# Kernel tuning notes

Hardware: AMD Instinct MI355X
Metric: run time of the kernel (lower is better)

## Reference

```python
import jax, jax.numpy as jnp
import numpy as np

T, C, H, W = 4, 512, 14, 14
NH, HD, N = 8, 64, H * W  # heads, head_dim, tokens
EPS = 1e-5
SG_ALPHA = 4.0  # spikingjelly default sigmoid surrogate alpha


@jax.custom_vjp
def heaviside_sg(u):
    return (u >= 0.0).astype(u.dtype)

def _hs_fwd(u):
    return heaviside_sg(u), u

def _hs_bwd(u, g):
    s = jax.nn.sigmoid(SG_ALPHA * u)
    return (g * SG_ALPHA * s * (1.0 - s),)

heaviside_sg.defvjp(_hs_fwd, _hs_bwd)


def lif(x, tau=2.0, v_th=1.0):
    """Multi-step LIF over leading time dim; hard reset to 0, detach_reset."""
    def step(v, xt):
        v = v + (xt - v) / tau
        s = heaviside_sg(v - v_th)
        v = v * (1.0 - jax.lax.stop_gradient(s))
        return v, s
    _, spikes = jax.lax.scan(step, jnp.zeros_like(x[0]), x)
    return spikes


def conv1x1_bn(x, w, gamma, beta, mean, var, bias=None):
    # x: [T,C,H,W]; 1x1 conv == channel matmul, then eval-mode BN
    y = jnp.einsum('tchw,oc->tohw', x, w)
    if bias is not None:
        y = y + bias[None, :, None, None]
    scale = gamma / jnp.sqrt(var + EPS)
    return y * scale[None, :, None, None] + (beta - mean * scale)[None, :, None, None]


def to_heads(y):
    # [T,C,H,W] -> [T, NH, N, HD]
    return y.reshape(T, C, N).transpose(0, 2, 1).reshape(T, N, NH, HD).transpose(0, 2, 1, 3)


def setup_inputs() -> dict:
    key = jax.random.key(0)
    ks = jax.random.split(key, 6)
    d = {
        'x': jax.random.normal(ks[0], (T, C, H, W), jnp.float32),
        'q_w': jax.random.normal(ks[1], (C, C), jnp.float32) * 0.05,
        'k_w': jax.random.normal(ks[2], (C, C), jnp.float32) * 0.05,
        'v_w': jax.random.normal(ks[3], (C, C), jnp.float32) * 0.05,
        'proj_w': jax.random.normal(ks[4], (C, C), jnp.float32) * 0.05,
        'proj_b': jnp.zeros((C,), jnp.float32),
    }
    for p in ('q', 'k', 'v', 'proj'):
        d[p + '_gamma'] = jnp.ones((C,), jnp.float32)
        d[p + '_beta'] = jnp.zeros((C,), jnp.float32)
        d[p + '_mean'] = jnp.zeros((C,), jnp.float32)
        d[p + '_var'] = jnp.ones((C,), jnp.float32)
    return d


def reference(x, q_w, q_gamma, q_beta, q_mean, q_var,
              k_w, k_gamma, k_beta, k_mean, k_var,
              v_w, v_gamma, v_beta, v_mean, v_var,
              proj_w, proj_b, proj_gamma, proj_beta, proj_mean, proj_var):
    identity = x
    xs = lif(x)  # shortcut_lif

    q = to_heads(lif(conv1x1_bn(xs, q_w, q_gamma, q_beta, q_mean, q_var)))  # [T,NH,N,HD]
    k = to_heads(lif(conv1x1_bn(xs, k_w, k_gamma, k_beta, k_mean, k_var)))
    v = to_heads(lif(conv1x1_bn(xs, v_w, v_gamma, v_beta, v_mean, v_var)))

    kv = (k * v).sum(axis=2, keepdims=True)        # [T,NH,1,HD] linear attention reduce
    kv = lif(kv, v_th=0.5)                          # talking_heads_lif
    attn = q * kv                                   # [T,NH,N,HD]

    y = attn.transpose(0, 1, 3, 2).reshape(T, C, H, W)
    out = conv1x1_bn(y, proj_w, proj_gamma, proj_beta, proj_mean, proj_var, bias=proj_b)
    return out + identity
```

## Files before the change

kernel.cpp:

```cpp
#include <hip/hip_runtime.h>


#define TT 4
#define CC 512
#define NN 196
#define BEPS 1e-5f

#define WQT_OFF 0
#define WKT_OFF (512 * 512)
#define WVT_OFF (2 * 512 * 512)
#define WPT_OFF (3 * 512 * 512)
#define KV_OFF  (4 * 512 * 512)
#define SQ_OFF  (4 * 512 * 512 + 2048)

__global__ __launch_bounds__(256) void k0_prep(
    const float* __restrict__ qw, const float* __restrict__ kw,
    const float* __restrict__ vw, const float* __restrict__ pw,
    float* __restrict__ ws)
{
    __shared__ float tile[64][65];
    const int b   = blockIdx.x;
    const int mat = b >> 6;
    const int t6  = b & 63;
    const int to  = (t6 >> 3) * 64;
    const int tc  = (t6 & 7) * 64;
    const float* W = (mat == 0) ? qw : (mat == 1) ? kw : (mat == 2) ? vw : pw;
    float* Wt = ws + (size_t)mat * (512 * 512);
    const int lr = threadIdx.x >> 6;
    const int lc = threadIdx.x & 63;
#pragma unroll
    for (int i = 0; i < 16; ++i) {
        int r = i * 4 + lr;
        tile[r][lc] = W[(size_t)(to + r) * 512 + (tc + lc)];
    }
    __syncthreads();
#pragma unroll
    for (int i = 0; i < 16; ++i) {
        int r = i * 4 + lr;
        Wt[(size_t)(tc + r) * 512 + (to + lc)] = tile[lc][r];
    }
    if (b == 0) {
        for (int i = threadIdx.x; i < TT * CC; i += 256) ws[KV_OFF + i] = 0.0f;
    }
}

__device__ __forceinline__ int bn_lif4(const float* acc, float sc, float of, float vth) {
    float v = 0.0f;
    int bits = 0;
#pragma unroll
    for (int t = 0; t < TT; ++t) {
        float y = acc[t] * sc + of;
        v = v + (y - v) * 0.5f;
        if (v >= vth) { bits |= (1 << t); v = 0.0f; }
    }
    return bits;
}

__device__ __forceinline__ void compact_append(int flag, int ch, int lane,
                                               unsigned short* actrow, int* cntp)
{
    unsigned long long m = __ballot(flag);
    int base = 0;
    if (lane == 0 && m) base = atomicAdd(cntp, __popcll(m));
    base = __shfl(base, 0);
    if (flag) actrow[base + __popcll(m & ((1ull << lane) - 1ull))] = (unsigned short)ch;
}

__global__ __launch_bounds__(512) void ka_qkv(
    const float* __restrict__ x, float* __restrict__ ws,
    const float* __restrict__ qg, const float* __restrict__ qb,
    const float* __restrict__ qm, const float* __restrict__ qv,
    const float* __restrict__ kg, const float* __restrict__ kb,
    const float* __restrict__ km, const float* __restrict__ kvv,
    const float* __restrict__ vg, const float* __restrict__ vb,
    const float* __restrict__ vm, const float* __restrict__ vvv)
{
    const int n    = blockIdx.x;
    const int tid  = threadIdx.x;
    const int lane = tid & 63;
    const int wave = tid >> 6;
    __shared__ unsigned short act[TT][CC];
    __shared__ int cnt[TT];
    if (tid < TT) cnt[tid] = 0;

    int xf = 0;
    {
        float v = 0.0f;
#pragma unroll
        for (int t = 0; t < TT; ++t) {
            float a = x[(size_t)(t * CC + tid) * NN + n];
            v = v + (a - v) * 0.5f;
            if (v >= 1.0f) { xf |= (1 << t); v = 0.0f; }
        }
    }
    __syncthreads();
#pragma unroll
    for (int t = 0; t < TT; ++t)
        compact_append((xf >> t) & 1, tid, lane, act[t], &cnt[t]);
    __syncthreads();

    int ct[TT];
    int mc = 0;
#pragma unroll
    for (int t = 0; t < TT; ++t) { ct[t] = cnt[t]; mc = max(mc, ct[t]); }

    float aq[TT] = {0,0,0,0}, ak[TT] = {0,0,0,0}, av[TT] = {0,0,0,0};
    const float* Wqt = ws + WQT_OFF;
    const float* Wkt = ws + WKT_OFF;
    const float* Wvt = ws + WVT_OFF;
    for (int i = 0; i < mc; ++i) {
#pragma unroll
        for (int t = 0; t < TT; ++t) {
            if (i < ct[t]) {
                const int c = act[t][i];
                aq[t] += Wqt[(size_t)c * CC + tid];
                ak[t] += Wkt[(size_t)c * CC + tid];
                av[t] += Wvt[(size_t)c * CC + tid];
            }
        }
    }

    int sqb, skb, svb;
    {
        float sc = qg[tid] / sqrtf(qv[tid] + BEPS);
        sqb = bn_lif4(aq, sc, qb[tid] - qm[tid] * sc, 1.0f);
        sc = kg[tid] / sqrtf(kvv[tid] + BEPS);
        skb = bn_lif4(ak, sc, kb[tid] - km[tid] * sc, 1.0f);
        sc = vg[tid] / sqrtf(vvv[tid] + BEPS);
        svb = bn_lif4(av, sc, vb[tid] - vm[tid] * sc, 1.0f);
    }

    unsigned* sqg = (unsigned*)(ws + SQ_OFF);
    float* kvsum = ws + KV_OFF;
#pragma unroll
    for (int t = 0; t < TT; ++t) {
        unsigned long long m = __ballot((sqb >> t) & 1);
        if (lane == 0) {
            sqg[((size_t)t * NN + n) * 16 + wave * 2]     = (unsigned)(m & 0xffffffffULL);
            sqg[((size_t)t * NN + n) * 16 + wave * 2 + 1] = (unsigned)(m >> 32);
        }
        if (((skb >> t) & 1) && ((svb >> t) & 1)) atomicAdd(&kvsum[t * CC + tid], 1.0f);
    }
}

__global__ __launch_bounds__(512) void kb_proj(
    const float* __restrict__ x, const float* __restrict__ ws,
    const float* __restrict__ pbias,
    const float* __restrict__ pg, const float* __restrict__ pb,
    const float* __restrict__ pm, const float* __restrict__ pv,
    float* __restrict__ out)
{
    const int n    = blockIdx.x;
    const int tid  = threadIdx.x;
    const int lane = tid & 63;
    __shared__ unsigned short act[TT][CC];
    __shared__ int cnt[TT];
    if (tid < TT) cnt[tid] = 0;

    const float* kvsum = ws + KV_OFF;
    const unsigned* sqg = (const unsigned*)(ws + SQ_OFF);

    int f = 0;
    {
        float v = 0.0f;
#pragma unroll
        for (int t = 0; t < TT; ++t) {
            float a = kvsum[t * CC + tid];
            v = v + (a - v) * 0.5f;
            const int s = (v >= 0.5f);
            if (s) v = 0.0f;
            const unsigned w = sqg[((size_t)t * NN + n) * 16 + (tid >> 5)];
            if (s && ((w >> (tid & 31)) & 1)) f |= (1 << t);
        }
    }
    __syncthreads();
#pragma unroll
    for (int t = 0; t < TT; ++t)
        compact_append((f >> t) & 1, tid, lane, act[t], &cnt[t]);
    __syncthreads();

    int ct[TT];
    int mc = 0;
#pragma unroll
    for (int t = 0; t < TT; ++t) { ct[t] = cnt[t]; mc = max(mc, ct[t]); }

    float a[TT] = {0,0,0,0};
    const float* Wpt = ws + WPT_OFF;
    for (int i = 0; i < mc; ++i) {
#pragma unroll
        for (int t = 0; t < TT; ++t) {
            if (i < ct[t]) {
                const int c = act[t][i];
                a[t] += Wpt[(size_t)c * CC + tid];
            }
        }
    }

    {
        const float sc = pg[tid] / sqrtf(pv[tid] + BEPS);
        const float of = pb[tid] - pm[tid] * sc;
        const float bi = pbias[tid];
#pragma unroll
        for (int t = 0; t < TT; ++t) {
            const size_t i0 = (size_t)(t * CC + tid) * NN + n;
            out[i0] = (a[t] + bi) * sc + of + x[i0];
        }
    }
}

extern "C" void kernel_launch(void* const* d_in, const int* in_sizes, int n_in,
                              void* d_out, int out_size, void* d_ws, size_t ws_size,
                              hipStream_t stream) {
    const float* x     = (const float*)d_in[0];
    const float* qw    = (const float*)d_in[1];
    const float* kw    = (const float*)d_in[2];
    const float* vw    = (const float*)d_in[3];
    const float* pw    = (const float*)d_in[4];
    const float* pbias = (const float*)d_in[5];
    const float* qg = (const float*)d_in[6],  *qb = (const float*)d_in[7];
    const float* qm = (const float*)d_in[8],  *qv = (const float*)d_in[9];
    const float* kg = (const float*)d_in[10], *kb = (const float*)d_in[11];
    const float* km = (const float*)d_in[12], *kv = (const float*)d_in[13];
    const float* vg = (const float*)d_in[14], *vb = (const float*)d_in[15];
    const float* vm = (const float*)d_in[16], *vv = (const float*)d_in[17];
    const float* pg = (const float*)d_in[18], *pb = (const float*)d_in[19];
    const float* pm = (const float*)d_in[20], *pv = (const float*)d_in[21];
    float* ws  = (float*)d_ws;
    float* out = (float*)d_out;

    hipLaunchKernelGGL(k0_prep, dim3(256), dim3(256), 0, stream, qw, kw, vw, pw, ws);
    hipLaunchKernelGGL(ka_qkv, dim3(196), dim3(512), 0, stream, x, ws,
                       qg, qb, qm, qv, kg, kb, km, kv, vg, vb, vm, vv);
    hipLaunchKernelGGL(kb_proj, dim3(196), dim3(512), 0, stream, x, ws,
                       pbias, pg, pb, pm, pv, out);
}
```

Before: 131.3 us.

## Fuse prep, QKV and projection kernels into one cooperative kernel with grid syncs

Merges the weight-transpose prep, QKV spike accumulation and projection kernels into one cooperative launch of 196 blocks, separated by grid-wide barriers. This removes two kernel launch boundaries and lets each block keep its Q spike bits in registers instead of writing and re-reading a global bitmask. In exchange the weight transposes are spread over 196 blocks of 512 threads, and the kernel depends on cooperative-launch residency and two grid.sync barriers.

```diff
diff --git a/kernel.cpp b/kernel.cpp
--- a/kernel.cpp
+++ b/kernel.cpp
@@ -1,4 +1,7 @@
 #include <hip/hip_runtime.h>
+#include <hip/hip_cooperative_groups.h>
+
+namespace cg = cooperative_groups;
 
 
 #define TT 4
@@ -11,47 +14,15 @@
 #define WVT_OFF (2 * 512 * 512)
 #define WPT_OFF (3 * 512 * 512)
 #define KV_OFF  (4 * 512 * 512)
-#define SQ_OFF  (4 * 512 * 512 + 2048)
-
-__global__ __launch_bounds__(256) void k0_prep(
-    const float* __restrict__ qw, const float* __restrict__ kw,
-    const float* __restrict__ vw, const float* __restrict__ pw,
-    float* __restrict__ ws)
-{
-    __shared__ float tile[64][65];
-    const int b   = blockIdx.x;
-    const int mat = b >> 6;
-    const int t6  = b & 63;
-    const int to  = (t6 >> 3) * 64;
-    const int tc  = (t6 & 7) * 64;
-    const float* W = (mat == 0) ? qw : (mat == 1) ? kw : (mat == 2) ? vw : pw;
-    float* Wt = ws + (size_t)mat * (512 * 512);
-    const int lr = threadIdx.x >> 6;
-    const int lc = threadIdx.x & 63;
-#pragma unroll
-    for (int i = 0; i < 16; ++i) {
-        int r = i * 4 + lr;
-        tile[r][lc] = W[(size_t)(to + r) * 512 + (tc + lc)];
-    }
-    __syncthreads();
-#pragma unroll
-    for (int i = 0; i < 16; ++i) {
-        int r = i * 4 + lr;
-        Wt[(size_t)(tc + r) * 512 + (to + lc)] = tile[lc][r];
-    }
-    if (b == 0) {
-        for (int i = threadIdx.x; i < TT * CC; i += 256) ws[KV_OFF + i] = 0.0f;
-    }
-}
-
-__device__ __forceinline__ int bn_lif4(const float* acc, float sc, float of, float vth) {
+
+__device__ __forceinline__ int bn_lif4(const float* acc, float sc, float of) {
     float v = 0.0f;
     int bits = 0;
 #pragma unroll
     for (int t = 0; t < TT; ++t) {
         float y = acc[t] * sc + of;
         v = v + (y - v) * 0.5f;
-        if (v >= vth) { bits |= (1 << t); v = 0.0f; }
+        if (v >= 1.0f) { bits |= (1 << t); v = 0.0f; }
     }
     return bits;
 }
@@ -66,29 +37,67 @@
     if (flag) actrow[base + __popcll(m & ((1ull << lane) - 1ull))] = (unsigned short)ch;
 }
 
-__global__ __launch_bounds__(512) void ka_qkv(
-    const float* __restrict__ x, float* __restrict__ ws,
+__global__ __launch_bounds__(512) void fused_ssa(
+    const float* __restrict__ x,
+    const float* __restrict__ qw, const float* __restrict__ kw,
+    const float* __restrict__ vw, const float* __restrict__ pw,
+    const float* __restrict__ pbias,
     const float* __restrict__ qg, const float* __restrict__ qb,
     const float* __restrict__ qm, const float* __restrict__ qv,
     const float* __restrict__ kg, const float* __restrict__ kb,
     const float* __restrict__ km, const float* __restrict__ kvv,
     const float* __restrict__ vg, const float* __restrict__ vb,
-    const float* __restrict__ vm, const float* __restrict__ vvv)
+    const float* __restrict__ vm, const float* __restrict__ vvv,
+    const float* __restrict__ pg, const float* __restrict__ pb,
+    const float* __restrict__ pm, const float* __restrict__ pv,
+    float* __restrict__ ws, float* __restrict__ out)
 {
-    const int n    = blockIdx.x;
+    cg::grid_group grid = cg::this_grid();
+    const int b    = blockIdx.x;
     const int tid  = threadIdx.x;
     const int lane = tid & 63;
-    const int wave = tid >> 6;
+
+    __shared__ float tile[64][65];
     __shared__ unsigned short act[TT][CC];
     __shared__ int cnt[TT];
+
+    {
+        const int lr = tid >> 6;
+        const int lc = tid & 63;
+        for (int job = b; job < 256; job += 196) {
+            const int mat = job >> 6;
+            const int t6  = job & 63;
+            const int to  = (t6 >> 3) * 64;
+            const int tc  = (t6 & 7) * 64;
+            const float* W = (mat == 0) ? qw : (mat == 1) ? kw : (mat == 2) ? vw : pw;
+            float* Wt = ws + (size_t)mat * (512 * 512);
+#pragma unroll
+            for (int i = 0; i < 8; ++i) {
+                const int r = i * 8 + lr;
+                tile[r][lc] = W[(size_t)(to + r) * 512 + (tc + lc)];
+            }
+            __syncthreads();
+#pragma unroll
+            for (int i = 0; i < 8; ++i) {
+                const int r = i * 8 + lr;
+                Wt[(size_t)(tc + r) * 512 + (to + lc)] = tile[lc][r];
+            }
+            __syncthreads();
+        }
+        if (b < TT) ws[KV_OFF + b * CC + tid] = 0.0f;
+    }
+    grid.sync();
+
+    const int n = b;
     if (tid < TT) cnt[tid] = 0;
 
     int xf = 0;
     {
         float v = 0.0f;
+        const float* xp = x + (size_t)tid * NN + n;
 #pragma unroll
         for (int t = 0; t < TT; ++t) {
-            float a = x[(size_t)(t * CC + tid) * NN + n];
+            const float a = xp[(size_t)t * CC * NN];
             v = v + (a - v) * 0.5f;
             if (v >= 1.0f) { xf |= (1 << t); v = 0.0f; }
         }
@@ -99,78 +108,60 @@
         compact_append((xf >> t) & 1, tid, lane, act[t], &cnt[t]);
     __syncthreads();
 
-    int ct[TT];
-    int mc = 0;
+    int ct[TT], mc = 0;
 #pragma unroll
     for (int t = 0; t < TT; ++t) { ct[t] = cnt[t]; mc = max(mc, ct[t]); }
 
     float aq[TT] = {0,0,0,0}, ak[TT] = {0,0,0,0}, av[TT] = {0,0,0,0};
-    const float* Wqt = ws + WQT_OFF;
-    const float* Wkt = ws + WKT_OFF;
-    const float* Wvt = ws + WVT_OFF;
-    for (int i = 0; i < mc; ++i) {
+    {
+        const float* Wqt = ws + WQT_OFF;
+        const float* Wkt = ws + WKT_OFF;
+        const float* Wvt = ws + WVT_OFF;
+        for (int i = 0; i < mc; ++i) {
+#pragma unroll
+            for (int t = 0; t < TT; ++t) {
+                if (i < ct[t]) {
+                    const int c = act[t][i];
+                    aq[t] += Wqt[(size_t)c * CC + tid];
+                    ak[t] += Wkt[(size_t)c * CC + tid];
+                    av[t] += Wvt[(size_t)c * CC + tid];
+                }
+            }
+        }
+    }
+
+    int sqb, skb, svb;
+    {
+        float sc = qg[tid] / sqrtf(qv[tid] + BEPS);
+        sqb = bn_lif4(aq, sc, qb[tid] - qm[tid] * sc);
+        sc = kg[tid] / sqrtf(kvv[tid] + BEPS);
+        skb = bn_lif4(ak, sc, kb[tid] - km[tid] * sc);
+        sc = vg[tid] / sqrtf(vvv[tid] + BEPS);
+        svb = bn_lif4(av, sc, vb[tid] - vm[tid] * sc);
+    }
+
+    {
+        float* kvsum = ws + KV_OFF;
+        const int both = skb & svb;
+#pragma unroll
+        for (int t = 0; t < TT; ++t)
+            if ((both >> t) & 1) atomicAdd(&kvsum[t * CC + tid], 1.0f);
+    }
+    grid.sync();
+
+    if (tid < TT) cnt[tid] = 0;
+
+    int f = 0;
+    {
+        const float* kvsum = ws + KV_OFF;
+        float v = 0.0f;
 #pragma unroll
         for (int t = 0; t < TT; ++t) {
-            if (i < ct[t]) {
-                const int c = act[t][i];
-                aq[t] += Wqt[(size_t)c * CC + tid];
-                ak[t] += Wkt[(size_t)c * CC + tid];
-                av[t] += Wvt[(size_t)c * CC + tid];
-            }
-        }
-    }
-
-    int sqb, skb, svb;
-    {
-        float sc = qg[tid] / sqrtf(qv[tid] + BEPS);
-        sqb = bn_lif4(aq, sc, qb[tid] - qm[tid] * sc, 1.0f);
-        sc = kg[tid] / sqrtf(kvv[tid] + BEPS);
-        skb = bn_lif4(ak, sc, kb[tid] - km[tid] * sc, 1.0f);
-        sc = vg[tid] / sqrtf(vvv[tid] + BEPS);
-        svb = bn_lif4(av, sc, vb[tid] - vm[tid] * sc, 1.0f);
-    }
-
-    unsigned* sqg = (unsigned*)(ws + SQ_OFF);
-    float* kvsum = ws + KV_OFF;
-#pragma unroll
-    for (int t = 0; t < TT; ++t) {
-        unsigned long long m = __ballot((sqb >> t) & 1);
-        if (lane == 0) {
-            sqg[((size_t)t * NN + n) * 16 + wave * 2]     = (unsigned)(m & 0xffffffffULL);
-            sqg[((size_t)t * NN + n) * 16 + wave * 2 + 1] = (unsigned)(m >> 32);
-        }
-        if (((skb >> t) & 1) && ((svb >> t) & 1)) atomicAdd(&kvsum[t * CC + tid], 1.0f);
-    }
-}
-
-__global__ __launch_bounds__(512) void kb_proj(
-    const float* __restrict__ x, const float* __restrict__ ws,
-    const float* __restrict__ pbias,
-    const float* __restrict__ pg, const float* __restrict__ pb,
-    const float* __restrict__ pm, const float* __restrict__ pv,
-    float* __restrict__ out)
-{
-    const int n    = blockIdx.x;
-    const int tid  = threadIdx.x;
-    const int lane = tid & 63;
-    __shared__ unsigned short act[TT][CC];
-    __shared__ int cnt[TT];
-    if (tid < TT) cnt[tid] = 0;
-
-    const float* kvsum = ws + KV_OFF;
-    const unsigned* sqg = (const unsigned*)(ws + SQ_OFF);
-
-    int f = 0;
-    {
-        float v = 0.0f;
-#pragma unroll
-        for (int t = 0; t < TT; ++t) {
-            float a = kvsum[t * CC + tid];
+            const float a = kvsum[t * CC + tid];
             v = v + (a - v) * 0.5f;
             const int s = (v >= 0.5f);
             if (s) v = 0.0f;
-            const unsigned w = sqg[((size_t)t * NN + n) * 16 + (tid >> 5)];
-            if (s && ((w >> (tid & 31)) & 1)) f |= (1 << t);
+            if (s && ((sqb >> t) & 1)) f |= (1 << t);
         }
     }
     __syncthreads();
@@ -179,19 +170,20 @@
         compact_append((f >> t) & 1, tid, lane, act[t], &cnt[t]);
     __syncthreads();
 
-    int ct[TT];
-    int mc = 0;
+    mc = 0;
 #pragma unroll
     for (int t = 0; t < TT; ++t) { ct[t] = cnt[t]; mc = max(mc, ct[t]); }
 
     float a[TT] = {0,0,0,0};
-    const float* Wpt = ws + WPT_OFF;
-    for (int i = 0; i < mc; ++i) {
-#pragma unroll
-        for (int t = 0; t < TT; ++t) {
-            if (i < ct[t]) {
-                const int c = act[t][i];
-                a[t] += Wpt[(size_t)c * CC + tid];
+    {
+        const float* Wpt = ws + WPT_OFF;
+        for (int i = 0; i < mc; ++i) {
+#pragma unroll
+            for (int t = 0; t < TT; ++t) {
+                if (i < ct[t]) {
+                    const int c = act[t][i];
+                    a[t] += Wpt[(size_t)c * CC + tid];
+                }
             }
         }
     }
@@ -228,9 +220,14 @@
     float* ws  = (float*)d_ws;
     float* out = (float*)d_out;
 
-    hipLaunchKernelGGL(k0_prep, dim3(256), dim3(256), 0, stream, qw, kw, vw, pw, ws);
-    hipLaunchKernelGGL(ka_qkv, dim3(196), dim3(512), 0, stream, x, ws,
-                       qg, qb, qm, qv, kg, kb, km, kv, vg, vb, vm, vv);
-    hipLaunchKernelGGL(kb_proj, dim3(196), dim3(512), 0, stream, x, ws,
-                       pbias, pg, pb, pm, pv, out);
-}
+    void* args[] = {
+        (void*)&x, (void*)&qw, (void*)&kw, (void*)&vw, (void*)&pw, (void*)&pbias,
+        (void*)&qg, (void*)&qb, (void*)&qm, (void*)&qv,
+        (void*)&kg, (void*)&kb, (void*)&km, (void*)&kv,
+        (void*)&vg, (void*)&vb, (void*)&vm, (void*)&vv,
+        (void*)&pg, (void*)&pb, (void*)&pm, (void*)&pv,
+        (void*)&ws, (void*)&out
+    };
+    hipLaunchCooperativeKernel((const void*)fused_ssa, dim3(196), dim3(512),
+                               args, 0, stream);
+}
```

After: 207.8 us. +58.3%, slower.
